# Kernel optimization log

Hardware: AMD Instinct MI355X
Metric: run time of the kernel (lower is better)

The kernel has to match this reference:

```python
import jax, jax.numpy as jnp
import numpy as np

B, T, H = 16, 512, 768
S = 32            # gold spans per example
L = 50            # max_span_len -> candidate ends per span
NT = 3            # num_types
HS = 4 * H        # span repr size


def setup_inputs() -> dict:
    key = jax.random.key(0)
    ks = jax.random.split(key, 8)
    h = jax.random.normal(ks[0], (B, T, H), dtype=jnp.float32)
    attention_mask = jnp.ones((B, T), dtype=jnp.int32)
    starts = jax.random.randint(ks[1], (B, S), 1, 400).astype(jnp.int32)
    lens = jax.random.randint(ks[2], (B, S), 0, L).astype(jnp.int32)
    ends = starts + lens                      # <= 448 < last_tok=510
    types = jax.random.randint(ks[3], (B, S), 0, NT).astype(jnp.int32)
    W1 = jax.random.normal(ks[4], (HS, HS), dtype=jnp.float32) * (1.0 / np.sqrt(HS))
    b1 = jnp.zeros((HS,), dtype=jnp.float32)
    w_score = jax.random.normal(ks[5], (HS,), dtype=jnp.float32) * (1.0 / np.sqrt(HS))
    b_score = jnp.zeros((1,), dtype=jnp.float32)
    W_type = jax.random.normal(ks[6], (HS, NT), dtype=jnp.float32) * (1.0 / np.sqrt(HS))
    b_type = jnp.zeros((NT,), dtype=jnp.float32)
    return {"h": h, "attention_mask": attention_mask, "span_starts": starts,
            "span_ends": ends, "span_types": types, "W1": W1, "b1": b1,
            "w_score": w_score, "b_score": b_score, "W_type": W_type, "b_type": b_type}


def _span_loss(h, attention_mask, span_starts, span_ends, span_types,
               W1, b1, w_score, b_score, W_type, b_type, type_loss_weight=1.0):
    cls = h[:, 0]                                              # [B,H]
    # prefix sums for O(1) segment means: pre[b,t] = sum h[b,0:t]
    pre = jnp.concatenate([jnp.zeros((B, 1, H), h.dtype), jnp.cumsum(h, axis=1)], axis=1)

    valid_len = attention_mask.sum(axis=1)                     # [B]
    last_tok = jnp.maximum(1, valid_len - 2)                   # [B]

    s = span_starts                                            # [B,S]
    e_gold = span_ends
    gold_idx = e_gold - s                                      # [B,S]
    lt = last_tok[:, None]
    span_valid = (s >= 1) & (s <= lt) & (e_gold >= s) & (e_gold <= lt) & (gold_idx < L)

    e_max = jnp.minimum(s + L - 1, lt)                         # [B,S]
    p = s[..., None] + jnp.arange(L, dtype=s.dtype)            # [B,S,L] candidate ends
    cand_valid = p <= e_max[..., None]

    sc = jnp.clip(s, 0, T - 1)
    pc = jnp.clip(p, 0, T - 1)
    bi2 = jnp.arange(B)[:, None]
    bi3 = jnp.arange(B)[:, None, None]

    h_start = h[bi2, sc]                                       # [B,S,H]
    h_end = h[bi3, pc]                                         # [B,S,L,H]
    seg_len = jnp.maximum(p - s[..., None] + 1, 1).astype(h.dtype)
    h_mean = (pre[bi3, pc + 1] - pre[bi2, sc][:, :, None]) / seg_len[..., None]

    repr_ = jnp.concatenate([
        jnp.broadcast_to(h_start[:, :, None], (B, S, L, H)),
        h_end,
        h_mean,
        jnp.broadcast_to(cls[:, None, None], (B, S, L, H)),
    ], axis=-1)                                                # [B,S,L,4H]

    h1 = jax.nn.gelu(jnp.einsum('bslh,hd->bsld', repr_, W1) + b1, approximate=False)
    scores = jnp.einsum('bsld,d->bsl', h1, w_score) + b_score[0]      # [B,S,L]
    type_logits = jnp.einsum('bsld,dk->bslk', h1, W_type) + b_type    # [B,S,L,NT]

    # end-index CE over valid candidate ends
    masked = jnp.where(cand_valid, scores, jnp.float32(-1e9))
    logp_end = jax.nn.log_softmax(masked, axis=-1)             # [B,S,L]
    gi = jnp.clip(gold_idx, 0, L - 1)
    end_loss = -jnp.take_along_axis(logp_end, gi[..., None], axis=-1)[..., 0]  # [B,S]

    # type CE at the gold end index
    tl_gold = jnp.take_along_axis(type_logits, gi[..., None, None], axis=2)[:, :, 0]  # [B,S,NT]
    logp_t = jax.nn.log_softmax(tl_gold, axis=-1)
    tg = jnp.clip(span_types, 0, NT - 1)
    type_loss = -jnp.take_along_axis(logp_t, tg[..., None], axis=-1)[..., 0]  # [B,S]

    vmask = span_valid.astype(h.dtype)
    n_seg = vmask.sum()
    denom = jnp.maximum(n_seg, 1.0)
    loss_end = jnp.where(n_seg > 0, (end_loss * vmask).sum() / denom, 0.0)
    loss_type = jnp.where(n_seg > 0, (type_loss * vmask).sum() / denom, 0.0)
    return loss_end + type_loss_weight * loss_type


def reference(h, attention_mask, span_starts, span_ends, span_types,
              W1, b1, w_score, b_score, W_type, b_type):
    return _span_loss(h, attention_mask, span_starts, span_ends, span_types,
                      W1, b1, w_score, b_score, W_type, b_type)
```

## Files before the change

kernel.cpp:

```cpp
#include <hip/hip_runtime.h>
#include <hip/hip_bf16.h>
#include <math.h>

#define B_ 16
#define T_ 512
#define H_ 768
#define S_ 32
#define L_ 50
#define NT_ 3
#define HS_ 3072
#define CH_ 32
#define CT_ 16

#define TX_ 464
#define YB2 7424
#define GB 14848
#define CLSB 15360
#define XYROWS 14848
#define AROWS 15616
#define NKT 24
#define SLOT_SH 16384

typedef __attribute__((ext_vector_type(8))) short short8;
typedef __attribute__((ext_vector_type(4))) float f32x4;

__device__ __forceinline__ unsigned short f2bf(float f) {
    __hip_bfloat16 b = __float2bfloat16(f);
    return *(unsigned short*)&b;
}
__device__ __forceinline__ float bf2f(unsigned short u) {
    union { unsigned int i; float f; } v; v.i = ((unsigned int)u) << 16; return v.f;
}
__device__ __forceinline__ void load_lds16(const void* g, void* l) {
    __builtin_amdgcn_global_load_lds((__attribute__((address_space(1))) void*)g,
                                     (__attribute__((address_space(3))) void*)l, 16, 0, 0);
}
__device__ __forceinline__ ushort4 pack4(float4 v) {
    ushort4 o; o.x = f2bf(v.x); o.y = f2bf(v.y); o.z = f2bf(v.z); o.w = f2bf(v.w);
    return o;
}

__device__ __forceinline__ float gelu_exact(float v) {
    float a = fabsf(v) * 0.70710678118654752f;
    float t = __builtin_amdgcn_rcpf(fmaf(a, 0.47047f, 1.0f));
    float poly = t * fmaf(t, fmaf(t, 0.7478556f, -0.0958798f), 0.3480242f);
    float e = __builtin_amdgcn_exp2f(a * a * -1.4426950408889634f);
    float erfa = fmaf(-poly, e, 1.0f);
    float erfv = copysignf(erfa, v);
    return 0.5f * v * (1.0f + erfv);
}

__global__ __launch_bounds__(256) void cumsum_pass1(const float4* __restrict__ h4,
                                                    float4* __restrict__ partial) {
    int idx = blockIdx.x * 256 + threadIdx.x;
    int hd4 = idx % 192; int t = idx / 192; int ch = t % CH_; int b = t / CH_;
    const float4* hp = h4 + ((size_t)b * T_ + ch * CT_) * 192 + hd4;
    float4 acc = {0.f, 0.f, 0.f, 0.f};
#pragma unroll
    for (int tt = 0; tt < CT_; tt++) {
        float4 v = hp[(size_t)tt * 192];
        acc.x += v.x; acc.y += v.y; acc.z += v.z; acc.w += v.w;
    }
    partial[idx] = acc;
}

__global__ __launch_bounds__(256) void cumsum_pass3(const float4* __restrict__ h4,
                                                    const float4* __restrict__ partial,
                                                    ushort4* __restrict__ Ab4) {
    int idx = blockIdx.x * 256 + threadIdx.x;
    int hd4 = idx % 192; int t = idx / 192; int ch = t % CH_; int b = t / CH_;
    if (ch * CT_ >= TX_) return;
    float4 acc = {0.f, 0.f, 0.f, 0.f};
#pragma unroll
    for (int c = 0; c < CH_; c++) {
        if (c < ch) {
            float4 v = partial[((size_t)b * CH_ + c) * 192 + hd4];
            acc.x += v.x; acc.y += v.y; acc.z += v.z; acc.w += v.w;
        }
    }
    const float4* hp = h4 + ((size_t)b * T_ + ch * CT_) * 192 + hd4;
    if (ch == 0) {
        ushort4 z = {0, 0, 0, 0};
        Ab4[((size_t)(YB2 + b * TX_)) * 192 + hd4] = z;
    }
#pragma unroll
    for (int tt = 0; tt < CT_; tt++) {
        int t2 = ch * CT_ + tt;
        float4 hv = hp[(size_t)tt * 192];
        if (t2 < TX_)
            Ab4[((size_t)(b * TX_ + t2)) * 192 + hd4] = pack4(hv);
        acc.x += hv.x; acc.y += hv.y; acc.z += hv.z; acc.w += hv.w;
        if (t2 + 1 < TX_)
            Ab4[((size_t)(YB2 + b * TX_ + t2 + 1)) * 192 + hd4] = pack4(acc);
    }
}

__global__ void gather_kernel(const float* __restrict__ h,
                              const int* __restrict__ starts,
                              __hip_bfloat16* __restrict__ Ab) {
    int r = blockIdx.x;
    int src_row, dst_row;
    if (r < B_ * S_) {
        int b = r / S_;
        int sv = starts[r];
        int sc = min(max(sv, 0), T_ - 1);
        src_row = b * T_ + sc;
        dst_row = GB + r;
    } else {
        int b = r - B_ * S_;
        src_row = b * T_;
        dst_row = CLSB + b;
    }
    __hip_bfloat16* dst = Ab + (size_t)dst_row * H_;
    const float* src = h + (size_t)src_row * H_;
    for (int j = threadIdx.x; j < H_; j += 256)
        dst[j] = __float2bfloat16(src[j]);
}

__global__ __launch_bounds__(256) void transpose_w(const float* __restrict__ W1,
                                                   __hip_bfloat16* __restrict__ Wt) {
    __shared__ float tile[64][65];
    int n0 = blockIdx.x * 64, k0 = blockIdx.y * 64;
    int c = threadIdx.x & 63, r0 = threadIdx.x >> 6;
#pragma unroll
    for (int i = 0; i < 16; i++) {
        int r = r0 + i * 4;
        tile[r][c] = W1[(size_t)(k0 + r) * HS_ + n0 + c];
    }
    __syncthreads();
    int p = k0 / H_, kl = k0 % H_;
    __hip_bfloat16* out = Wt + (size_t)p * HS_ * H_;
#pragma unroll
    for (int i = 0; i < 16; i++) {
        int r = r0 + i * 4;
        out[(size_t)(n0 + r) * H_ + kl + c] = __float2bfloat16(tile[c][r]);
    }
}

__device__ __forceinline__ void stage_tile(const __hip_bfloat16* __restrict__ Ab,
                                           const __hip_bfloat16* __restrict__ Bt,
                                           short* slot, int m0, int n0, int k0, int tid) {
    int wave = tid >> 6;
    int row = tid >> 2;
    int c8 = (tid & 3) * 8;
    const __hip_bfloat16* ap = Ab + (size_t)(m0 + row) * H_ + k0 + c8;
    const __hip_bfloat16* bp = Bt + (size_t)(n0 + row) * H_ + k0 + c8;
    char* la = (char*)slot + wave * 1024;
    char* lb = (char*)(slot + 8192) + wave * 1024;
    load_lds16(ap, la);
    load_lds16(ap + (size_t)128 * H_, la + 8192);
    load_lds16(bp, lb);
    load_lds16(bp + (size_t)128 * H_, lb + 8192);
}

__device__ __forceinline__ void compute_tile(const short* __restrict__ As,
                                             f32x4 (&acc)[8][4],
                                             int rA, int rB, int kgo) {
    const short* Bs = As + 8192;
    short8 a0[4], a1[4], bfr[4];
#pragma unroll
    for (int f = 0; f < 4; ++f)
        a0[f] = *(const short8*)&As[(rA + f * 16) * 32 + kgo];
#pragma unroll
    for (int f = 0; f < 4; ++f)
        bfr[f] = *(const short8*)&Bs[(rB + f * 16) * 32 + kgo];
#pragma unroll
    for (int f = 0; f < 4; ++f)
        a1[f] = *(const short8*)&As[(rA + 64 + f * 16) * 32 + kgo];
    __builtin_amdgcn_s_setprio(1);
#pragma unroll
    for (int mf = 0; mf < 4; ++mf)
#pragma unroll
        for (int nf = 0; nf < 4; ++nf)
            acc[mf][nf] = __builtin_amdgcn_mfma_f32_16x16x32_bf16(
                a0[mf], bfr[nf], acc[mf][nf], 0, 0, 0);
    __builtin_amdgcn_s_setprio(0);
    __builtin_amdgcn_s_setprio(1);
#pragma unroll
    for (int mf = 0; mf < 4; ++mf)
#pragma unroll
        for (int nf = 0; nf < 4; ++nf)
            acc[4 + mf][nf] = __builtin_amdgcn_mfma_f32_16x16x32_bf16(
                a1[mf], bfr[nf], acc[4 + mf][nf], 0, 0, 0);
    __builtin_amdgcn_s_setprio(0);
}

__global__ __launch_bounds__(512, 2) void mfma_gemm(const __hip_bfloat16* __restrict__ Ab,
                                                    const __hip_bfloat16* __restrict__ Wt,
                                                    __hip_bfloat16* __restrict__ XY,
                                                    float* __restrict__ ST,
                                                    float* __restrict__ CC) {
    __shared__ short lds[4 * SLOT_SH];
    int tid = threadIdx.x;
    int wave = tid >> 6, lane = tid & 63;
    int wr = wave >> 2, wc = wave & 3;

    int orig = blockIdx.x;
    int xcd = orig & 7, loc = orig >> 3;
    int wg = (xcd < 4 ? xcd * 92 : 368 + (xcd - 4) * 91) + loc;
    int mt = wg / 12, nt = wg - mt * 12;
    int m0 = mt << 8, n0 = nt << 8;

    const __hip_bfloat16* Bt;
    if (m0 < YB2)        Bt = Wt + (size_t)1 * HS_ * H_;
    else if (m0 < GB)    Bt = Wt + (size_t)2 * HS_ * H_;
    else if (m0 < CLSB)  Bt = Wt;
    else                 Bt = Wt + (size_t)3 * HS_ * H_;

    f32x4 acc[8][4] = {};

    for (int t = 0; t < 3; ++t)
        stage_tile(Ab, Bt, lds + t * SLOT_SH, m0, n0, t * 32, tid);

    int l15 = lane & 15;
    int kgo = (lane >> 4) * 8;
    int rA = wr * 128 + l15;
    int rB = wc * 64 + l15;

    for (int kt = 0; kt < NKT - 3; ++kt) {
        asm volatile("s_waitcnt vmcnt(8)" ::: "memory");
        __builtin_amdgcn_s_barrier();
        __builtin_amdgcn_sched_barrier(0);
        stage_tile(Ab, Bt, lds + ((kt + 3) & 3) * SLOT_SH, m0, n0, (kt + 3) * 32, tid);
        compute_tile(lds + (kt & 3) * SLOT_SH, acc, rA, rB, kgo);
        __builtin_amdgcn_sched_barrier(0);
    }
    asm volatile("s_waitcnt vmcnt(8)" ::: "memory");
    __builtin_amdgcn_s_barrier();
    __builtin_amdgcn_sched_barrier(0);
    compute_tile(lds + ((NKT - 3) & 3) * SLOT_SH, acc, rA, rB, kgo);
    __builtin_amdgcn_sched_barrier(0);
    asm volatile("s_waitcnt vmcnt(4)" ::: "memory");
    __builtin_amdgcn_s_barrier();
    __builtin_amdgcn_sched_barrier(0);
    compute_tile(lds + ((NKT - 2) & 3) * SLOT_SH, acc, rA, rB, kgo);
    __builtin_amdgcn_sched_barrier(0);
    asm volatile("s_waitcnt vmcnt(0)" ::: "memory");
    __builtin_amdgcn_s_barrier();
    __builtin_amdgcn_sched_barrier(0);
    compute_tile(lds + ((NKT - 1) & 3) * SLOT_SH, acc, rA, rB, kgo);

    int mb = m0 + wr * 128, nb = n0 + wc * 64;
#pragma unroll
    for (int mf = 0; mf < 8; ++mf) {
#pragma unroll
        for (int nf = 0; nf < 4; ++nf) {
            int n = nb + nf * 16 + l15;
            int mr = mb + mf * 16 + (lane >> 4) * 4;
#pragma unroll
            for (int r = 0; r < 4; ++r) {
                int m = mr + r;
                float v = acc[mf][nf][r];
                if (m < XYROWS) {
                    XY[(size_t)m * HS_ + n] = __float2bfloat16(v);
                } else if (m < CLSB) {
                    ST[(size_t)(m - GB) * HS_ + n] = v;
                } else if (m < CLSB + 16) {
                    CC[(size_t)(m - CLSB) * HS_ + n] = v;
                }
            }
        }
    }
}

__global__ __launch_bounds__(256) void c0_kernel(const float4* __restrict__ ST,
                                                 const float4* __restrict__ CC,
                                                 const float4* __restrict__ b1,
                                                 const float4* __restrict__ w_score,
                                                 ushort4* __restrict__ c0b,
                                                 ushort4* __restrict__ wb16) {
    if (blockIdx.x >= 512 * HS_ / 4 / 256) {
        int i = (blockIdx.x - 512 * HS_ / 4 / 256) * 256 + threadIdx.x;
        wb16[i] = pack4(w_score[i]);
        return;
    }
    int i = blockIdx.x * 256 + threadIdx.x;
    int row = i / (HS_ / 4);
    int b = row >> 5;
    int c4 = i % (HS_ / 4);
    float4 s = ST[i], c = CC[b * (HS_ / 4) + c4], bb = b1[c4];
    float4 v = {s.x + c.x + bb.x, s.y + c.y + bb.y, s.z + c.z + bb.z, s.w + c.w + bb.w};
    c0b[i] = pack4(v);
}

__global__ __launch_bounds__(256) void combine_kernel(
    const unsigned short* __restrict__ c0, const unsigned short* __restrict__ wb16,
    const __hip_bfloat16* __restrict__ XY,
    const float* __restrict__ b_score, const float* __restrict__ W_type,
    const int* __restrict__ starts, const int* __restrict__ ends,
    float* __restrict__ scores, float* __restrict__ tgold) {
    int x = blockIdx.x;
    int b = x & 15, s = x >> 4;
    int bs = b * S_ + s;
    int wave = threadIdx.x >> 6, lane = threadIdx.x & 63;
    int pr = blockIdx.y * 4 + wave;
    if (pr >= L_ / 2) return;
    int l0 = pr * 2, l1 = l0 + 1;
    int sv = starts[bs], ev = ends[bs];
    int gi = min(max(ev - sv, 0), L_ - 1);
    int sc = min(max(sv, 0), TX_ - 1);
    int pc0 = min(max(sv + l0, 0), TX_ - 2);
    int pc1 = min(max(sv + l1, 0), TX_ - 2);
    float inv0 = 1.0f / (float)(l0 + 1);
    float inv1 = 1.0f / (float)(l1 + 1);
    bool isg0 = (l0 == gi), isg1 = (l1 == gi);
    bool anyg = isg0 || isg1;

    const unsigned short* X0 = (const unsigned short*)(XY + (size_t)(b * TX_ + pc0) * HS_);
    const unsigned short* X1 = (const unsigned short*)(XY + (size_t)(b * TX_ + pc1) * HS_);
    const unsigned short* Y0 = (const unsigned short*)(XY + (size_t)(YB2 + b * TX_ + pc0 + 1) * HS_);
    const unsigned short* Y1 = (const unsigned short*)(XY + (size_t)(YB2 + b * TX_ + pc1 + 1) * HS_);
    const unsigned short* Ysr = (const unsigned short*)(XY + (size_t)(YB2 + b * TX_ + sc) * HS_);
    const unsigned short* c0r = c0 + (size_t)bs * HS_;

    float local0 = 0.f, local1 = 0.f, t0 = 0.f, t1 = 0.f, t2 = 0.f;
#pragma unroll
    for (int j = 0; j < 6; j++) {
        int d = j * 512 + lane * 8;
        short8 xv0 = *(const short8*)(X0 + d);
        short8 xv1 = *(const short8*)(X1 + d);
        short8 yv0 = *(const short8*)(Y0 + d);
        short8 yv1 = *(const short8*)(Y1 + d);
        short8 sv8 = *(const short8*)(Ysr + d);
        short8 cv8 = *(const short8*)(c0r + d);
        short8 wv8 = *(const short8*)(wb16 + d);
#pragma unroll
        for (int q = 0; q < 8; q++) {
            float ys = bf2f(((const unsigned short*)&sv8)[q]);
            float cv = bf2f(((const unsigned short*)&cv8)[q]);
            float w  = bf2f(((const unsigned short*)&wv8)[q]);
            float v0 = fmaf(bf2f(((const unsigned short*)&yv0)[q]) - ys, inv0, cv) +
                       bf2f(((const unsigned short*)&xv0)[q]);
            float v1 = fmaf(bf2f(((const unsigned short*)&yv1)[q]) - ys, inv1, cv) +
                       bf2f(((const unsigned short*)&xv1)[q]);
            float g0 = gelu_exact(v0);
            float g1 = gelu_exact(v1);
            local0 = fmaf(g0, w, local0);
            local1 = fmaf(g1, w, local1);
            if (anyg) {
                float gg = isg0 ? g0 : g1;
                t0 = fmaf(gg, W_type[(d + q) * NT_ + 0], t0);
                t1 = fmaf(gg, W_type[(d + q) * NT_ + 1], t1);
                t2 = fmaf(gg, W_type[(d + q) * NT_ + 2], t2);
            }
        }
    }
#pragma unroll
    for (int off = 32; off >= 1; off >>= 1) {
        local0 += __shfl_down(local0, off);
        local1 += __shfl_down(local1, off);
    }
    if (lane == 0) {
        float bs0 = b_score[0];
        scores[(size_t)bs * L_ + l0] = local0 + bs0;
        scores[(size_t)bs * L_ + l1] = local1 + bs0;
    }
    if (anyg) {
#pragma unroll
        for (int off = 32; off >= 1; off >>= 1) {
            t0 += __shfl_down(t0, off);
            t1 += __shfl_down(t1, off);
            t2 += __shfl_down(t2, off);
        }
        if (lane == 0) {
            tgold[bs * NT_ + 0] = t0;
            tgold[bs * NT_ + 1] = t1;
            tgold[bs * NT_ + 2] = t2;
        }
    }
}

__global__ __launch_bounds__(512) void loss_kernel(
    const float* __restrict__ scores, const float* __restrict__ tgold,
    const int* __restrict__ mask, const int* __restrict__ starts,
    const int* __restrict__ ends, const int* __restrict__ types,
    const float* __restrict__ b_type, float* __restrict__ out) {
    __shared__ int svl[B_];
    __shared__ float r[3][8];
    int tid = threadIdx.x;
    int b = tid / S_;
    if (tid < B_) svl[tid] = 0;
    __syncthreads();
    {
        int part = 0;
        const int* mp = mask + tid * 16;
#pragma unroll
        for (int i = 0; i < 16; i++) part += mp[i];
        atomicAdd(&svl[tid / (T_ / 16)], part);
    }
    __syncthreads();
    int vl = svl[b];
    int lt = max(1, vl - 2);
    int sv = starts[tid], ev = ends[tid];
    int gold = ev - sv;
    bool valid = (sv >= 1) && (sv <= lt) && (ev >= sv) && (ev <= lt) && (gold < L_);
    int emax = min(sv + L_ - 1, lt);
    const float* sp = scores + (size_t)tid * L_;
    float m = -1e30f;
    for (int l = 0; l < L_; l++) {
        float v = (sv + l <= emax) ? sp[l] : -1e9f;
        m = fmaxf(m, v);
    }
    float sum = 0.f;
    for (int l = 0; l < L_; l++) {
        float v = (sv + l <= emax) ? sp[l] : -1e9f;
        sum += expf(v - m);
    }
    int gi = min(max(gold, 0), L_ - 1);
    float vg = (sv + gi <= emax) ? sp[gi] : -1e9f;
    float end_loss = (m + logf(sum)) - vg;

    float t0 = tgold[tid * 3 + 0] + b_type[0];
    float t1 = tgold[tid * 3 + 1] + b_type[1];
    float t2 = tgold[tid * 3 + 2] + b_type[2];
    float tm = fmaxf(t0, fmaxf(t1, t2));
    float tsum = expf(t0 - tm) + expf(t1 - tm) + expf(t2 - tm);
    int tg = min(max(types[tid], 0), NT_ - 1);
    float tv = (tg == 0) ? t0 : ((tg == 1) ? t1 : t2);
    float type_loss = (tm + logf(tsum)) - tv;

    float ve = valid ? end_loss : 0.f;
    float vt = valid ? type_loss : 0.f;
    float vc = valid ? 1.f : 0.f;
    for (int off = 32; off >= 1; off >>= 1) {
        ve += __shfl_down(ve, off);
        vt += __shfl_down(vt, off);
        vc += __shfl_down(vc, off);
    }
    if ((tid & 63) == 0) {
        int w = tid >> 6;
        r[0][w] = ve; r[1][w] = vt; r[2][w] = vc;
    }
    __syncthreads();
    if (tid == 0) {
        float se = 0, st = 0, n = 0;
        for (int w = 0; w < 8; w++) { se += r[0][w]; st += r[1][w]; n += r[2][w]; }
        float denom = fmaxf(n, 1.f);
        out[0] = (n > 0.f) ? (se / denom + st / denom) : 0.f;
    }
}

extern "C" void kernel_launch(void* const* d_in, const int* in_sizes, int n_in,
                              void* d_out, int out_size, void* d_ws, size_t ws_size,
                              hipStream_t stream) {
    const float* h       = (const float*)d_in[0];
    const int*   mask    = (const int*)d_in[1];
    const int*   starts  = (const int*)d_in[2];
    const int*   ends    = (const int*)d_in[3];
    const int*   types   = (const int*)d_in[4];
    const float* W1      = (const float*)d_in[5];
    const float* b1      = (const float*)d_in[6];
    const float* w_score = (const float*)d_in[7];
    const float* b_score = (const float*)d_in[8];
    const float* W_type  = (const float*)d_in[9];
    const float* b_type  = (const float*)d_in[10];
    float* out = (float*)d_out;

    char* ws = (char*)d_ws;
    size_t off = 0;
    __hip_bfloat16* Ab = (__hip_bfloat16*)(ws + off); off += (size_t)AROWS * H_ * 2;
    __hip_bfloat16* XY = (__hip_bfloat16*)(ws + off); off += (size_t)XYROWS * HS_ * 2;
    __hip_bfloat16* Wt = (__hip_bfloat16*)(ws + off); off += (size_t)4 * HS_ * H_ * 2;
    float* ST     = (float*)(ws + off);               off += (size_t)512 * HS_ * 4;
    float* CC     = (float*)(ws + off);               off += (size_t)16 * HS_ * 4;
    unsigned short* c0b = (unsigned short*)(ws + off); off += (size_t)512 * HS_ * 2;
    unsigned short* wb16 = (unsigned short*)(ws + off); off += (size_t)HS_ * 2;
    float* scores = (float*)(ws + off);               off += (size_t)B_ * S_ * L_ * 4;
    float* tgold  = (float*)(ws + off);               off += (size_t)B_ * S_ * NT_ * 4;
    float4* partial = (float4*)XY;

    hipLaunchKernelGGL(cumsum_pass1, dim3(B_ * CH_ * 192 / 256), dim3(256), 0, stream,
                       (const float4*)h, partial);
    hipLaunchKernelGGL(cumsum_pass3, dim3(B_ * CH_ * 192 / 256), dim3(256), 0, stream,
                       (const float4*)h, (const float4*)partial, (ushort4*)Ab);
    hipLaunchKernelGGL(gather_kernel, dim3(B_ * S_ + B_), dim3(256), 0, stream, h, starts, Ab);
    hipLaunchKernelGGL(transpose_w, dim3(48, 48), dim3(256), 0, stream, W1, Wt);
    hipLaunchKernelGGL(mfma_gemm, dim3((AROWS / 256) * 12), dim3(512), 0, stream,
                       Ab, Wt, XY, ST, CC);
    hipLaunchKernelGGL(c0_kernel, dim3(512 * HS_ / 4 / 256 + 3), dim3(256), 0, stream,
                       (const float4*)ST, (const float4*)CC, (const float4*)b1,
                       (const float4*)w_score, (ushort4*)c0b, (ushort4*)wb16);
    hipLaunchKernelGGL(combine_kernel, dim3(B_ * S_, 7), dim3(256), 0, stream,
                       c0b, wb16, XY, b_score, W_type, starts, ends, scores, tgold);
    hipLaunchKernelGGL(loss_kernel, dim3(1), dim3(512), 0, stream,
                       scores, tgold, mask, starts, ends, types, b_type, out);
}
```

Baseline: 319.0 us.

## Swizzle LDS layout and interleave staging with split MFMA phases

```diff
diff --git a/kernel.cpp b/kernel.cpp
--- a/kernel.cpp
+++ b/kernel.cpp
@@ -137,53 +137,59 @@
     }
 }
 
-__device__ __forceinline__ void stage_tile(const __hip_bfloat16* __restrict__ Ab,
-                                           const __hip_bfloat16* __restrict__ Bt,
-                                           short* slot, int m0, int n0, int k0, int tid) {
-    int wave = tid >> 6;
-    int row = tid >> 2;
-    int c8 = (tid & 3) * 8;
-    const __hip_bfloat16* ap = Ab + (size_t)(m0 + row) * H_ + k0 + c8;
-    const __hip_bfloat16* bp = Bt + (size_t)(n0 + row) * H_ + k0 + c8;
-    char* la = (char*)slot + wave * 1024;
-    char* lb = (char*)(slot + 8192) + wave * 1024;
-    load_lds16(ap, la);
-    load_lds16(ap + (size_t)128 * H_, la + 8192);
-    load_lds16(bp, lb);
-    load_lds16(bp + (size_t)128 * H_, lb + 8192);
-}
-
-__device__ __forceinline__ void compute_tile(const short* __restrict__ As,
-                                             f32x4 (&acc)[8][4],
-                                             int rA, int rB, int kgo) {
-    const short* Bs = As + 8192;
-    short8 a0[4], a1[4], bfr[4];
-#pragma unroll
-    for (int f = 0; f < 4; ++f)
-        a0[f] = *(const short8*)&As[(rA + f * 16) * 32 + kgo];
-#pragma unroll
-    for (int f = 0; f < 4; ++f)
-        bfr[f] = *(const short8*)&Bs[(rB + f * 16) * 32 + kgo];
-#pragma unroll
-    for (int f = 0; f < 4; ++f)
-        a1[f] = *(const short8*)&As[(rA + 64 + f * 16) * 32 + kgo];
-    __builtin_amdgcn_s_setprio(1);
+__device__ __forceinline__ void mfma16(const short8 (&a)[4], const short8 (&b)[4],
+                                       f32x4 (&acc)[8][4], int off) {
 #pragma unroll
     for (int mf = 0; mf < 4; ++mf)
 #pragma unroll
         for (int nf = 0; nf < 4; ++nf)
-            acc[mf][nf] = __builtin_amdgcn_mfma_f32_16x16x32_bf16(
-                a0[mf], bfr[nf], acc[mf][nf], 0, 0, 0);
-    __builtin_amdgcn_s_setprio(0);
-    __builtin_amdgcn_s_setprio(1);
-#pragma unroll
-    for (int mf = 0; mf < 4; ++mf)
-#pragma unroll
-        for (int nf = 0; nf < 4; ++nf)
-            acc[4 + mf][nf] = __builtin_amdgcn_mfma_f32_16x16x32_bf16(
-                a1[mf], bfr[nf], acc[4 + mf][nf], 0, 0, 0);
-    __builtin_amdgcn_s_setprio(0);
-}
+            acc[off + mf][nf] = __builtin_amdgcn_mfma_f32_16x16x32_bf16(
+                a[mf], b[nf], acc[off + mf][nf], 0, 0, 0);
+}
+
+#define STAGE_A(nslot, k0_) {                                                  \
+    char* d_ = (char*)(nslot) + dstoff;                                        \
+    load_lds16(pA + (k0_), d_);                                                \
+    load_lds16(pA + (size_t)128 * H_ + (k0_), d_ + 8192);                      \
+}
+#define STAGE_B(nslot, k0_) {                                                  \
+    char* d_ = (char*)(nslot) + 16384 + dstoff;                                \
+    load_lds16(pB + (k0_), d_);                                                \
+    load_lds16(pB + (size_t)128 * H_ + (k0_), d_ + 8192);                      \
+}
+
+#define TILE_STEP(kt, WAITSTR, DO_STAGE)                                       \
+  {                                                                            \
+    const short* slot = lds + ((kt) & 3) * SLOT_SH;                            \
+    short* nslot = lds + (((kt) + 3) & 3) * SLOT_SH;                           \
+    asm volatile(WAITSTR ::: "memory");                                        \
+    __builtin_amdgcn_s_barrier();                                              \
+    __builtin_amdgcn_sched_barrier(0);                                         \
+    short8 a[4], b[4];                                                         \
+    _Pragma("unroll")                                                          \
+    for (int i = 0; i < 4; ++i)                                                \
+      a[i] = *(const short8*)&slot[(wr * 128 + i * 16 + l15) * 32 + pcs];      \
+    _Pragma("unroll")                                                          \
+    for (int i = 0; i < 4; ++i)                                                \
+      b[i] = *(const short8*)&slot[8192 + (wc * 64 + i * 16 + l15) * 32 + pcs];\
+    if (DO_STAGE) { STAGE_A(nslot, ((kt) + 3) * 32) }                          \
+    asm volatile("s_waitcnt lgkmcnt(0)" ::: "memory");                         \
+    __builtin_amdgcn_sched_barrier(0);                                         \
+    __builtin_amdgcn_s_setprio(1);                                             \
+    mfma16(a, b, acc, 0);                                                      \
+    __builtin_amdgcn_s_setprio(0);                                             \
+    __builtin_amdgcn_s_barrier();                                              \
+    __builtin_amdgcn_sched_barrier(0);                                         \
+    _Pragma("unroll")                                                          \
+    for (int i = 0; i < 4; ++i)                                                \
+      a[i] = *(const short8*)&slot[(wr * 128 + 64 + i * 16 + l15) * 32 + pcs]; \
+    if (DO_STAGE) { STAGE_B(nslot, ((kt) + 3) * 32) }                          \
+    asm volatile("s_waitcnt lgkmcnt(0)" ::: "memory");                         \
+    __builtin_amdgcn_sched_barrier(0);                                         \
+    __builtin_amdgcn_s_setprio(1);                                             \
+    mfma16(a, b, acc, 4);                                                      \
+    __builtin_amdgcn_s_setprio(0);                                             \
+  }
 
 __global__ __launch_bounds__(512, 2) void mfma_gemm(const __hip_bfloat16* __restrict__ Ab,
                                                     const __hip_bfloat16* __restrict__ Wt,
@@ -194,6 +200,8 @@
     int tid = threadIdx.x;
     int wave = tid >> 6, lane = tid & 63;
     int wr = wave >> 2, wc = wave & 3;
+    int l15 = lane & 15;
+    int pcs = ((lane >> 4) ^ ((l15 >> 1) & 3)) * 8;
 
     int orig = blockIdx.x;
     int xcd = orig & 7, loc = orig >> 3;
@@ -207,38 +215,25 @@
     else if (m0 < CLSB)  Bt = Wt;
     else                 Bt = Wt + (size_t)3 * HS_ * H_;
 
+    int srow = wave * 16 + (lane >> 2);
+    int lcS = ((lane & 3) ^ ((lane >> 3) & 3)) * 8;
+    const __hip_bfloat16* pA = Ab + (size_t)(m0 + srow) * H_ + lcS;
+    const __hip_bfloat16* pB = Bt + (size_t)(n0 + srow) * H_ + lcS;
+    int dstoff = wave * 1024;
+
     f32x4 acc[8][4] = {};
 
-    for (int t = 0; t < 3; ++t)
-        stage_tile(Ab, Bt, lds + t * SLOT_SH, m0, n0, t * 32, tid);
-
-    int l15 = lane & 15;
-    int kgo = (lane >> 4) * 8;
-    int rA = wr * 128 + l15;
-    int rB = wc * 64 + l15;
-
-    for (int kt = 0; kt < NKT - 3; ++kt) {
-        asm volatile("s_waitcnt vmcnt(8)" ::: "memory");
-        __builtin_amdgcn_s_barrier();
-        __builtin_amdgcn_sched_barrier(0);
-        stage_tile(Ab, Bt, lds + ((kt + 3) & 3) * SLOT_SH, m0, n0, (kt + 3) * 32, tid);
-        compute_tile(lds + (kt & 3) * SLOT_SH, acc, rA, rB, kgo);
-        __builtin_amdgcn_sched_barrier(0);
-    }
-    asm volatile("s_waitcnt vmcnt(8)" ::: "memory");
-    __builtin_amdgcn_s_barrier();
-    __builtin_amdgcn_sched_barrier(0);
-    compute_tile(lds + ((NKT - 3) & 3) * SLOT_SH, acc, rA, rB, kgo);
-    __builtin_amdgcn_sched_barrier(0);
-    asm volatile("s_waitcnt vmcnt(4)" ::: "memory");
-    __builtin_amdgcn_s_barrier();
-    __builtin_amdgcn_sched_barrier(0);
-    compute_tile(lds + ((NKT - 2) & 3) * SLOT_SH, acc, rA, rB, kgo);
-    __builtin_amdgcn_sched_barrier(0);
-    asm volatile("s_waitcnt vmcnt(0)" ::: "memory");
-    __builtin_amdgcn_s_barrier();
-    __builtin_amdgcn_sched_barrier(0);
-    compute_tile(lds + ((NKT - 1) & 3) * SLOT_SH, acc, rA, rB, kgo);
+#pragma unroll
+    for (int t = 0; t < 3; ++t) {
+        STAGE_A(lds + t * SLOT_SH, t * 32)
+        STAGE_B(lds + t * SLOT_SH, t * 32)
+    }
+
+    for (int kt = 0; kt < NKT - 3; ++kt)
+        TILE_STEP(kt, "s_waitcnt vmcnt(8)", true)
+    TILE_STEP(NKT - 3, "s_waitcnt vmcnt(8)", false)
+    TILE_STEP(NKT - 2, "s_waitcnt vmcnt(4)", false)
+    TILE_STEP(NKT - 1, "s_waitcnt vmcnt(0)", false)
 
     int mb = m0 + wr * 128, nb = n0 + wc * 64;
 #pragma unroll
```

After: 317.2 us. Within noise of the previous version (-0.6%).

## Shrink GEMM tile to 128x128 with double buffering and swizzled LDS layout

Applied to the files above, without the earlier changes.

```diff
diff --git a/kernel.cpp b/kernel.cpp
--- a/kernel.cpp
+++ b/kernel.cpp
@@ -19,7 +19,7 @@
 #define XYROWS 14848
 #define AROWS 15616
 #define NKT 24
-#define SLOT_SH 16384
+#define GSLOT 8192
 
 typedef __attribute__((ext_vector_type(8))) short short8;
 typedef __attribute__((ext_vector_type(4))) float f32x4;
@@ -137,69 +137,22 @@
     }
 }
 
-__device__ __forceinline__ void stage_tile(const __hip_bfloat16* __restrict__ Ab,
-                                           const __hip_bfloat16* __restrict__ Bt,
-                                           short* slot, int m0, int n0, int k0, int tid) {
-    int wave = tid >> 6;
-    int row = tid >> 2;
-    int c8 = (tid & 3) * 8;
-    const __hip_bfloat16* ap = Ab + (size_t)(m0 + row) * H_ + k0 + c8;
-    const __hip_bfloat16* bp = Bt + (size_t)(n0 + row) * H_ + k0 + c8;
-    char* la = (char*)slot + wave * 1024;
-    char* lb = (char*)(slot + 8192) + wave * 1024;
-    load_lds16(ap, la);
-    load_lds16(ap + (size_t)128 * H_, la + 8192);
-    load_lds16(bp, lb);
-    load_lds16(bp + (size_t)128 * H_, lb + 8192);
-}
-
-__device__ __forceinline__ void compute_tile(const short* __restrict__ As,
-                                             f32x4 (&acc)[8][4],
-                                             int rA, int rB, int kgo) {
-    const short* Bs = As + 8192;
-    short8 a0[4], a1[4], bfr[4];
-#pragma unroll
-    for (int f = 0; f < 4; ++f)
-        a0[f] = *(const short8*)&As[(rA + f * 16) * 32 + kgo];
-#pragma unroll
-    for (int f = 0; f < 4; ++f)
-        bfr[f] = *(const short8*)&Bs[(rB + f * 16) * 32 + kgo];
-#pragma unroll
-    for (int f = 0; f < 4; ++f)
-        a1[f] = *(const short8*)&As[(rA + 64 + f * 16) * 32 + kgo];
-    __builtin_amdgcn_s_setprio(1);
-#pragma unroll
-    for (int mf = 0; mf < 4; ++mf)
-#pragma unroll
-        for (int nf = 0; nf < 4; ++nf)
-            acc[mf][nf] = __builtin_amdgcn_mfma_f32_16x16x32_bf16(
-                a0[mf], bfr[nf], acc[mf][nf], 0, 0, 0);
-    __builtin_amdgcn_s_setprio(0);
-    __builtin_amdgcn_s_setprio(1);
-#pragma unroll
-    for (int mf = 0; mf < 4; ++mf)
-#pragma unroll
-        for (int nf = 0; nf < 4; ++nf)
-            acc[4 + mf][nf] = __builtin_amdgcn_mfma_f32_16x16x32_bf16(
-                a1[mf], bfr[nf], acc[4 + mf][nf], 0, 0, 0);
-    __builtin_amdgcn_s_setprio(0);
-}
-
-__global__ __launch_bounds__(512, 2) void mfma_gemm(const __hip_bfloat16* __restrict__ Ab,
+__global__ __launch_bounds__(256, 3) void mfma_gemm(const __hip_bfloat16* __restrict__ Ab,
                                                     const __hip_bfloat16* __restrict__ Wt,
                                                     __hip_bfloat16* __restrict__ XY,
                                                     float* __restrict__ ST,
                                                     float* __restrict__ CC) {
-    __shared__ short lds[4 * SLOT_SH];
+    __shared__ short lds[2 * GSLOT];
     int tid = threadIdx.x;
     int wave = tid >> 6, lane = tid & 63;
-    int wr = wave >> 2, wc = wave & 3;
+    int wr = wave >> 1, wc = wave & 1;
+    int l15 = lane & 15;
+    int pcs = ((lane >> 4) ^ ((l15 >> 1) & 3)) * 8;
 
     int orig = blockIdx.x;
-    int xcd = orig & 7, loc = orig >> 3;
-    int wg = (xcd < 4 ? xcd * 92 : 368 + (xcd - 4) * 91) + loc;
-    int mt = wg / 12, nt = wg - mt * 12;
-    int m0 = mt << 8, n0 = nt << 8;
+    int wg = (orig & 7) * 366 + (orig >> 3);
+    int mt = wg / 24, nt = wg - mt * 24;
+    int m0 = mt << 7, n0 = nt << 7;
 
     const __hip_bfloat16* Bt;
     if (m0 < YB2)        Bt = Wt + (size_t)1 * HS_ * H_;
@@ -207,50 +160,67 @@
     else if (m0 < CLSB)  Bt = Wt;
     else                 Bt = Wt + (size_t)3 * HS_ * H_;
 
-    f32x4 acc[8][4] = {};
-
-    for (int t = 0; t < 3; ++t)
-        stage_tile(Ab, Bt, lds + t * SLOT_SH, m0, n0, t * 32, tid);
-
-    int l15 = lane & 15;
-    int kgo = (lane >> 4) * 8;
-    int rA = wr * 128 + l15;
-    int rB = wc * 64 + l15;
-
-    for (int kt = 0; kt < NKT - 3; ++kt) {
-        asm volatile("s_waitcnt vmcnt(8)" ::: "memory");
+    int cid0 = wave * 128 + lane;
+    int cid1 = cid0 + 64;
+    int row0 = cid0 >> 2, row1 = cid1 >> 2;
+    int lc0 = ((cid0 & 3) ^ ((row0 >> 1) & 3)) * 8;
+    int lc1 = ((cid1 & 3) ^ ((row1 >> 1) & 3)) * 8;
+    const __hip_bfloat16* pA0 = Ab + (size_t)(m0 + row0) * H_ + lc0;
+    const __hip_bfloat16* pA1 = Ab + (size_t)(m0 + row1) * H_ + lc1;
+    const __hip_bfloat16* pB0 = Bt + (size_t)(n0 + row0) * H_ + lc0;
+    const __hip_bfloat16* pB1 = Bt + (size_t)(n0 + row1) * H_ + lc1;
+    int dstoff = wave * 2048;
+
+#define STAGE2(kt_) {                                                          \
+    char* da = (char*)lds + ((kt_) & 1) * (GSLOT * 2) + dstoff;                \
+    load_lds16(pA0 + (kt_) * 32, da);                                          \
+    load_lds16(pA1 + (kt_) * 32, da + 1024);                                   \
+    load_lds16(pB0 + (kt_) * 32, da + 8192);                                   \
+    load_lds16(pB1 + (kt_) * 32, da + 9216);                                   \
+}
+
+    f32x4 acc[4][4] = {};
+
+    STAGE2(0)
+
+    for (int kt = 0; kt < NKT; ++kt) {
+        const short* cur = lds + (kt & 1) * GSLOT;
+        if (kt + 1 < NKT) {
+            STAGE2(kt + 1)
+            asm volatile("s_waitcnt vmcnt(4)" ::: "memory");
+        } else {
+            asm volatile("s_waitcnt vmcnt(0)" ::: "memory");
+        }
         __builtin_amdgcn_s_barrier();
         __builtin_amdgcn_sched_barrier(0);
-        stage_tile(Ab, Bt, lds + ((kt + 3) & 3) * SLOT_SH, m0, n0, (kt + 3) * 32, tid);
-        compute_tile(lds + (kt & 3) * SLOT_SH, acc, rA, rB, kgo);
+        short8 a[4], b[4];
+#pragma unroll
+        for (int f = 0; f < 4; ++f)
+            a[f] = *(const short8*)&cur[(wr * 64 + f * 16 + l15) * 32 + pcs];
+#pragma unroll
+        for (int f = 0; f < 4; ++f)
+            b[f] = *(const short8*)&cur[4096 + (wc * 64 + f * 16 + l15) * 32 + pcs];
+#pragma unroll
+        for (int fm = 0; fm < 4; ++fm)
+#pragma unroll
+            for (int fn = 0; fn < 4; ++fn)
+                acc[fm][fn] = __builtin_amdgcn_mfma_f32_16x16x32_bf16(
+                    a[fm], b[fn], acc[fm][fn], 0, 0, 0);
         __builtin_amdgcn_sched_barrier(0);
-    }
-    asm volatile("s_waitcnt vmcnt(8)" ::: "memory");
-    __builtin_amdgcn_s_barrier();
-    __builtin_amdgcn_sched_barrier(0);
-    compute_tile(lds + ((NKT - 3) & 3) * SLOT_SH, acc, rA, rB, kgo);
-    __builtin_amdgcn_sched_barrier(0);
-    asm volatile("s_waitcnt vmcnt(4)" ::: "memory");
-    __builtin_amdgcn_s_barrier();
-    __builtin_amdgcn_sched_barrier(0);
-    compute_tile(lds + ((NKT - 2) & 3) * SLOT_SH, acc, rA, rB, kgo);
-    __builtin_amdgcn_sched_barrier(0);
-    asm volatile("s_waitcnt vmcnt(0)" ::: "memory");
-    __builtin_amdgcn_s_barrier();
-    __builtin_amdgcn_sched_barrier(0);
-    compute_tile(lds + ((NKT - 1) & 3) * SLOT_SH, acc, rA, rB, kgo);
-
-    int mb = m0 + wr * 128, nb = n0 + wc * 64;
-#pragma unroll
-    for (int mf = 0; mf < 8; ++mf) {
-#pragma unroll
-        for (int nf = 0; nf < 4; ++nf) {
-            int n = nb + nf * 16 + l15;
-            int mr = mb + mf * 16 + (lane >> 4) * 4;
+        __builtin_amdgcn_s_barrier();
+    }
+
+    int mb = m0 + wr * 64, nb = n0 + wc * 64;
+#pragma unroll
+    for (int fm = 0; fm < 4; ++fm) {
+#pragma unroll
+        for (int fn = 0; fn < 4; ++fn) {
+            int n = nb + fn * 16 + l15;
+            int mr = mb + fm * 16 + (lane >> 4) * 4;
 #pragma unroll
             for (int r = 0; r < 4; ++r) {
                 int m = mr + r;
-                float v = acc[mf][nf][r];
+                float v = acc[fm][fn][r];
                 if (m < XYROWS) {
                     XY[(size_t)m * HS_ + n] = __float2bfloat16(v);
                 } else if (m < CLSB) {
@@ -261,6 +231,7 @@
             }
         }
     }
+#undef STAGE2
 }
 
 __global__ __launch_bounds__(256) void c0_kernel(const float4* __restrict__ ST,
@@ -475,7 +446,7 @@
                        (const float4*)h, (const float4*)partial, (ushort4*)Ab);
     hipLaunchKernelGGL(gather_kernel, dim3(B_ * S_ + B_), dim3(256), 0, stream, h, starts, Ab);
     hipLaunchKernelGGL(transpose_w, dim3(48, 48), dim3(256), 0, stream, W1, Wt);
-    hipLaunchKernelGGL(mfma_gemm, dim3((AROWS / 256) * 12), dim3(512), 0, stream,
+    hipLaunchKernelGGL(mfma_gemm, dim3((AROWS / 128) * (HS_ / 128)), dim3(256), 0, stream,
                        Ab, Wt, XY, ST, CC);
     hipLaunchKernelGGL(c0_kernel, dim3(512 * HS_ / 4 / 256 + 3), dim3(256), 0, stream,
                        (const float4*)ST, (const float4*)CC, (const float4*)b1,
```

New measurement: 316.0 us. About the same (-0.9%).
